# Optimization experiments

Hardware: AMD Instinct MI355X
Metric: run time of the kernel (lower is better)

## Reference

```python
import jax, jax.numpy as jnp
import numpy as np

B, C, L = 128, 1, 4096


def setup_inputs() -> dict:
    key = jax.random.key(0)
    x_0 = jax.random.normal(key, (B, C, L), dtype=jnp.float32)
    return {"x_0": x_0}


def reference(x_0):
    # Original: per-sample F.conv1d(x, flip(x), padding=L-1).
    # Cross-correlation with a flipped kernel == full linear convolution:
    #   out[b, t] = sum_c sum_i x[b,c,i] * x[b,c,t-i],  t in [0, 2L-2]
    # Vectorized over batch and channels via vmap; summed over channels
    # (conv1d contracts input channels against the weight's channel dim).
    conv = jax.vmap(jax.vmap(lambda a: jnp.convolve(a, a, mode='full')))(x_0)  # [B, C, 2L-1]
    return conv.sum(axis=1)[:, None, :]  # [B, 1, 2L-1]
```

## Files before the change

### kernel.cpp

```cpp
#include <hip/hip_runtime.h>

#define LL    4096
#define OUTL  8191
#define FPAD  272
#define NPDW  2336
#define CB1   2352
#define RB    4704
#define BTOP  5887
#define LDSDW 9824

typedef short v8s __attribute__((ext_vector_type(8)));
typedef float v4f __attribute__((ext_vector_type(4)));

__device__ __forceinline__ unsigned bf16b(float f) {
    unsigned u = __builtin_bit_cast(unsigned, f);
    u += 0x7fff + ((u >> 16) & 1);
    return u >> 16;
}
__device__ __forceinline__ unsigned pk(float lo, float hi) {
    return bf16b(lo) | (bf16b(hi) << 16);
}
__device__ __forceinline__ int swz(int g) {
    return (g & ~15) | ((g & 1) << 3) | ((g & 15) >> 1);
}

struct Frag {
    unsigned x0, x1, x2, x3, y0, y1, y2, y3;
    uint4 b3, b2, b1, b0;
};

__global__ __launch_bounds__(512, 4)
void selfconv_mfma7(const float* __restrict__ xg, float* __restrict__ outg) {
    __shared__ unsigned lds[LDSDW];
    const int tid = threadIdx.x;
    const int blk = blockIdx.x;
    const int b   = blk & 127;
    const int id  = blk >> 7;
    const int rg  = (id == 0) ? 0 : (id == 1) ? 3 : (id == 2) ? 1 : 2;
    const int T0  = rg << 11;
    const float* __restrict__ xb = xg + b * LL;

#pragma unroll
    for (int rr = 0; rr < 2; ++rr) {
        int w = tid + rr * 512;
        if (w < 584) {
            int E = 8 * w - FPAD;
            float e0,e1,e2,e3,e4,e5,e6,e7,e8;
            if (E >= 0 && E + 8 < LL) {
                float4 fa = *(const float4*)(xb + E);
                float4 fb = *(const float4*)(xb + E + 4);
                e0=fa.x; e1=fa.y; e2=fa.z; e3=fa.w;
                e4=fb.x; e5=fb.y; e6=fb.z; e7=fb.w; e8=xb[E+8];
            } else {
                float t[9];
#pragma unroll
                for (int k = 0; k < 9; ++k) {
                    int e = E + k;
                    t[k] = (e >= 0 && e < LL) ? xb[e] : 0.f;
                }
                e0=t[0]; e1=t[1]; e2=t[2]; e3=t[3]; e4=t[4];
                e5=t[5]; e6=t[6]; e7=t[7]; e8=t[8];
            }
            uint4 d0{pk(e0,e1), pk(e2,e3), pk(e4,e5), pk(e6,e7)};
            uint4 d1{pk(e1,e2), pk(e3,e4), pk(e5,e6), pk(e7,e8)};
            *(uint4*)&lds[4 * w]       = d0;
            *(uint4*)&lds[CB1 + 4 * w] = d1;
        }
    }
    {
        int g = 224 + tid;
        int x0 = BTOP - 7 - 8 * g;
        float4 fa = *(const float4*)(xb + x0);
        float4 fb = *(const float4*)(xb + x0 + 4);
        uint4 o{pk(fb.w, fb.z), pk(fb.y, fb.x), pk(fa.w, fa.z), pk(fa.y, fa.x)};
        *(uint4*)&lds[RB + 4 * swz(g)] = o;
    }
    if (tid < 480) {
        int u = (tid < 224) ? tid : tid + 512;
        *(uint4*)&lds[RB + 4 * u] = uint4{0, 0, 0, 0};
    }
    __syncthreads();

    const int wv = tid >> 6, lane = tid & 63, ln16 = lane & 15, q = lane >> 4;

    int mn = 0x7fffffff, mx = -0x7fffffff;
#pragma unroll
    for (int u = 0; u < 2; ++u)
#pragma unroll
        for (int v = 0; v < 4; ++v) {
            int base = T0 + 256 * u + 512 * v;
            int iLo = base - (LL - 1); if (iLo < 0) iLo = 0;
            int iHi = base + 255;      if (iHi > LL - 1) iHi = LL - 1;
            int a = iLo - 256 * u; if (a < mn) mn = a;
            int c2 = iHi - 256 * u; if (c2 > mx) mx = c2;
        }
    const int base_   = mn - 15;
    const int i0start = base_ - ((base_ - 1) & 7);
    const int nch     = ((mx - i0start) >> 5) + 1;
    const int nw      = (nch - wv + 7) >> 3;
    const int i0w     = i0start + 32 * wv;

    const int s0p = i0w + ln16 + 8 * q + FPAD;
    const int aw  = (s0p >> 1) + ((s0p & 1) ? CB1 : 0);
    const int g3 = (4352 - T0 + i0w - 16 * ln16 + 8 * q) >> 3;
    const int bw = RB + 4 * swz(g3);

    v4f a00{0,0,0,0}, a01{0,0,0,0}, a02{0,0,0,0}, a03{0,0,0,0};
    v4f a10{0,0,0,0}, a11{0,0,0,0}, a12{0,0,0,0}, a13{0,0,0,0};

    auto ld = [&](Frag& F, int a, int w) {
        F.x0 = lds[a];       F.x1 = lds[a + 1];
        F.x2 = lds[a + 2];   F.x3 = lds[a + 3];
        F.y0 = lds[a + 128]; F.y1 = lds[a + 129];
        F.y2 = lds[a + 130]; F.y3 = lds[a + 131];
        F.b3 = *(const uint4*)&lds[w];
        F.b2 = *(const uint4*)&lds[w + 256];
        F.b1 = *(const uint4*)&lds[w + 512];
        F.b0 = *(const uint4*)&lds[w + 768];
    };
    auto mkA = [](unsigned u0, unsigned u1, unsigned u2, unsigned u3) {
        union { unsigned x[4]; v8s s; } z;
        z.x[0] = u0; z.x[1] = u1; z.x[2] = u2; z.x[3] = u3; return z.s;
    };
    auto mkB = [](uint4 v) {
        union { unsigned x[4]; v8s s; } z;
        z.x[0] = v.x; z.x[1] = v.y; z.x[2] = v.z; z.x[3] = v.w; return z.s;
    };
    auto cmp = [&](const Frag& F) {
        v8s A0 = mkA(F.x0, F.x1, F.x2, F.x3);
        v8s A1 = mkA(F.y0, F.y1, F.y2, F.y3);
        v8s B3 = mkB(F.b3), B2 = mkB(F.b2), B1 = mkB(F.b1), B0 = mkB(F.b0);
        a03 = __builtin_amdgcn_mfma_f32_16x16x32_bf16(A0, B3, a03, 0, 0, 0);
        a13 = __builtin_amdgcn_mfma_f32_16x16x32_bf16(A1, B3, a13, 0, 0, 0);
        a02 = __builtin_amdgcn_mfma_f32_16x16x32_bf16(A0, B2, a02, 0, 0, 0);
        a12 = __builtin_amdgcn_mfma_f32_16x16x32_bf16(A1, B2, a12, 0, 0, 0);
        a01 = __builtin_amdgcn_mfma_f32_16x16x32_bf16(A0, B1, a01, 0, 0, 0);
        a11 = __builtin_amdgcn_mfma_f32_16x16x32_bf16(A1, B1, a11, 0, 0, 0);
        a00 = __builtin_amdgcn_mfma_f32_16x16x32_bf16(A0, B0, a00, 0, 0, 0);
        a10 = __builtin_amdgcn_mfma_f32_16x16x32_bf16(A1, B0, a10, 0, 0, 0);
    };

    Frag F0, F1;
    int awE = aw, bwE = bw, awO = aw + 128, bwO = bw + 128;
    ld(F0, awE, bwE); awE += 256; bwE += 256;
    ld(F1, awO, bwO); awO += 256; bwO += 256;
    int c = 0;
    for (; c + 2 < nw; c += 2) {
        cmp(F0); ld(F0, awE, bwE); awE += 256; bwE += 256;
        cmp(F1); ld(F1, awO, bwO); awO += 256; bwO += 256;
    }
    cmp(F0);
    if (c + 1 < nw) cmp(F1);

    float* fs = (float*)lds;
    __syncthreads();
    if (wv >= 4) {
        int sb = (wv - 4) * 2304 + lane * 36;
        *(v4f*)&fs[sb]      = a00; *(v4f*)&fs[sb + 4]  = a10;
        *(v4f*)&fs[sb + 8]  = a01; *(v4f*)&fs[sb + 12] = a11;
        *(v4f*)&fs[sb + 16] = a02; *(v4f*)&fs[sb + 20] = a12;
        *(v4f*)&fs[sb + 24] = a03; *(v4f*)&fs[sb + 28] = a13;
    }
    __syncthreads();
    if (wv < 4) {
        int sb = wv * 2304 + lane * 36;
        a00 += *(const v4f*)&fs[sb];      a10 += *(const v4f*)&fs[sb + 4];
        a01 += *(const v4f*)&fs[sb + 8];  a11 += *(const v4f*)&fs[sb + 12];
        a02 += *(const v4f*)&fs[sb + 16]; a12 += *(const v4f*)&fs[sb + 20];
        a03 += *(const v4f*)&fs[sb + 24]; a13 += *(const v4f*)&fs[sb + 28];
    }
    __syncthreads();
    if (wv >= 1 && wv < 4) {
        int sb = (wv - 1) * 2304 + lane * 36;
        *(v4f*)&fs[sb]      = a00; *(v4f*)&fs[sb + 4]  = a10;
        *(v4f*)&fs[sb + 8]  = a01; *(v4f*)&fs[sb + 12] = a11;
        *(v4f*)&fs[sb + 16] = a02; *(v4f*)&fs[sb + 20] = a12;
        *(v4f*)&fs[sb + 24] = a03; *(v4f*)&fs[sb + 28] = a13;
    }
    __syncthreads();
    if (wv == 0) {
#pragma unroll
        for (int s = 0; s < 3; ++s) {
            int sb = s * 2304 + lane * 36;
            a00 += *(const v4f*)&fs[sb];      a10 += *(const v4f*)&fs[sb + 4];
            a01 += *(const v4f*)&fs[sb + 8];  a11 += *(const v4f*)&fs[sb + 12];
            a02 += *(const v4f*)&fs[sb + 16]; a12 += *(const v4f*)&fs[sb + 20];
            a03 += *(const v4f*)&fs[sb + 24]; a13 += *(const v4f*)&fs[sb + 28];
        }
        float* __restrict__ ob = outg + b * OUTL;
        const v4f* accs[8] = {&a00, &a10, &a01, &a11, &a02, &a12, &a03, &a13};
#pragma unroll
        for (int uv = 0; uv < 8; ++uv) {
            int u = uv & 1, v = uv >> 1;
            int tilebase = T0 + 256 * u + 512 * v;
            int tb = tilebase + 4 * q + 16 * ln16;
            v4f a = *accs[uv];
            if (tilebase + 255 < OUTL) {
                *(v4f*)&ob[tb] = a;
            } else {
#pragma unroll
                for (int r2 = 0; r2 < 4; ++r2)
                    if (tb + r2 < OUTL) ob[tb + r2] = a[r2];
            }
        }
    }
}

extern "C" void kernel_launch(void* const* d_in, const int* in_sizes, int n_in,
                              void* d_out, int out_size, void* d_ws, size_t ws_size,
                              hipStream_t stream) {
    const float* x = (const float*)d_in[0];
    float* out = (float*)d_out;
    selfconv_mfma7<<<dim3(512), dim3(512), 0, stream>>>(x, out);
}
```

Before: 61.95 us.

## Split output into 1024-wide ranges across 1024 blocks with fewer accumulators

Result: no change. 62.00 us (+0.1%).

```diff
diff --git a/kernel.cpp b/kernel.cpp
--- a/kernel.cpp
+++ b/kernel.cpp
@@ -5,9 +5,9 @@
 #define FPAD  272
 #define NPDW  2336
 #define CB1   2352
-#define RB    4704
+#define RB    4688
 #define BTOP  5887
-#define LDSDW 9824
+#define LDSDW 8656
 
 typedef short v8s __attribute__((ext_vector_type(8)));
 typedef float v4f __attribute__((ext_vector_type(4)));
@@ -24,20 +24,16 @@
     return (g & ~15) | ((g & 1) << 3) | ((g & 15) >> 1);
 }
 
-struct Frag {
-    unsigned x0, x1, x2, x3, y0, y1, y2, y3;
-    uint4 b3, b2, b1, b0;
-};
-
-__global__ __launch_bounds__(512, 4)
-void selfconv_mfma7(const float* __restrict__ xg, float* __restrict__ outg) {
+__global__ __launch_bounds__(512, 8)
+void selfconv_mfma8(const float* __restrict__ xg, float* __restrict__ outg) {
     __shared__ unsigned lds[LDSDW];
     const int tid = threadIdx.x;
     const int blk = blockIdx.x;
     const int b   = blk & 127;
     const int id  = blk >> 7;
-    const int rg  = (id == 0) ? 0 : (id == 1) ? 3 : (id == 2) ? 1 : 2;
-    const int T0  = rg << 11;
+    const int perm[8] = {0, 3, 1, 2, 5, 6, 4, 7};
+    const int rg  = perm[id];
+    const int T0  = rg << 10;
     const float* __restrict__ xb = xg + b * LL;
 
 #pragma unroll
@@ -87,7 +83,7 @@
 #pragma unroll
     for (int u = 0; u < 2; ++u)
 #pragma unroll
-        for (int v = 0; v < 4; ++v) {
+        for (int v = 0; v < 2; ++v) {
             int base = T0 + 256 * u + 512 * v;
             int iLo = base - (LL - 1); if (iLo < 0) iLo = 0;
             int iHi = base + 255;      if (iHi > LL - 1) iHi = LL - 1;
@@ -101,23 +97,12 @@
     const int i0w     = i0start + 32 * wv;
 
     const int s0p = i0w + ln16 + 8 * q + FPAD;
-    const int aw  = (s0p >> 1) + ((s0p & 1) ? CB1 : 0);
-    const int g3 = (4352 - T0 + i0w - 16 * ln16 + 8 * q) >> 3;
-    const int bw = RB + 4 * swz(g3);
+    int aw = (s0p >> 1) + ((s0p & 1) ? CB1 : 0);
+    const int g1 = (BTOP - T0 - 512 - 16 * ln16 + i0w + 8 * q) >> 3;
+    int bw = RB + 4 * swz(g1);
 
-    v4f a00{0,0,0,0}, a01{0,0,0,0}, a02{0,0,0,0}, a03{0,0,0,0};
-    v4f a10{0,0,0,0}, a11{0,0,0,0}, a12{0,0,0,0}, a13{0,0,0,0};
+    v4f a00{0,0,0,0}, a10{0,0,0,0}, a01{0,0,0,0}, a11{0,0,0,0};
 
-    auto ld = [&](Frag& F, int a, int w) {
-        F.x0 = lds[a];       F.x1 = lds[a + 1];
-        F.x2 = lds[a + 2];   F.x3 = lds[a + 3];
-        F.y0 = lds[a + 128]; F.y1 = lds[a + 129];
-        F.y2 = lds[a + 130]; F.y3 = lds[a + 131];
-        F.b3 = *(const uint4*)&lds[w];
-        F.b2 = *(const uint4*)&lds[w + 256];
-        F.b1 = *(const uint4*)&lds[w + 512];
-        F.b0 = *(const uint4*)&lds[w + 768];
-    };
     auto mkA = [](unsigned u0, unsigned u1, unsigned u2, unsigned u3) {
         union { unsigned x[4]; v8s s; } z;
         z.x[0] = u0; z.x[1] = u1; z.x[2] = u2; z.x[3] = u3; return z.s;
@@ -126,75 +111,57 @@
         union { unsigned x[4]; v8s s; } z;
         z.x[0] = v.x; z.x[1] = v.y; z.x[2] = v.z; z.x[3] = v.w; return z.s;
     };
-    auto cmp = [&](const Frag& F) {
-        v8s A0 = mkA(F.x0, F.x1, F.x2, F.x3);
-        v8s A1 = mkA(F.y0, F.y1, F.y2, F.y3);
-        v8s B3 = mkB(F.b3), B2 = mkB(F.b2), B1 = mkB(F.b1), B0 = mkB(F.b0);
-        a03 = __builtin_amdgcn_mfma_f32_16x16x32_bf16(A0, B3, a03, 0, 0, 0);
-        a13 = __builtin_amdgcn_mfma_f32_16x16x32_bf16(A1, B3, a13, 0, 0, 0);
-        a02 = __builtin_amdgcn_mfma_f32_16x16x32_bf16(A0, B2, a02, 0, 0, 0);
-        a12 = __builtin_amdgcn_mfma_f32_16x16x32_bf16(A1, B2, a12, 0, 0, 0);
+
+    for (int c = 0; c < nw; ++c) {
+        unsigned x0 = lds[aw],       x1 = lds[aw + 1];
+        unsigned x2 = lds[aw + 2],   x3 = lds[aw + 3];
+        unsigned y0 = lds[aw + 128], y1 = lds[aw + 129];
+        unsigned y2 = lds[aw + 130], y3 = lds[aw + 131];
+        uint4 bv1 = *(const uint4*)&lds[bw];
+        uint4 bv0 = *(const uint4*)&lds[bw + 256];
+        v8s A0 = mkA(x0, x1, x2, x3);
+        v8s A1 = mkA(y0, y1, y2, y3);
+        v8s B1 = mkB(bv1);
+        v8s B0 = mkB(bv0);
+        a00 = __builtin_amdgcn_mfma_f32_16x16x32_bf16(A0, B0, a00, 0, 0, 0);
+        a10 = __builtin_amdgcn_mfma_f32_16x16x32_bf16(A1, B0, a10, 0, 0, 0);
         a01 = __builtin_amdgcn_mfma_f32_16x16x32_bf16(A0, B1, a01, 0, 0, 0);
         a11 = __builtin_amdgcn_mfma_f32_16x16x32_bf16(A1, B1, a11, 0, 0, 0);
-        a00 = __builtin_amdgcn_mfma_f32_16x16x32_bf16(A0, B0, a00, 0, 0, 0);
-        a10 = __builtin_amdgcn_mfma_f32_16x16x32_bf16(A1, B0, a10, 0, 0, 0);
-    };
-
-    Frag F0, F1;
-    int awE = aw, bwE = bw, awO = aw + 128, bwO = bw + 128;
-    ld(F0, awE, bwE); awE += 256; bwE += 256;
-    ld(F1, awO, bwO); awO += 256; bwO += 256;
-    int c = 0;
-    for (; c + 2 < nw; c += 2) {
-        cmp(F0); ld(F0, awE, bwE); awE += 256; bwE += 256;
-        cmp(F1); ld(F1, awO, bwO); awO += 256; bwO += 256;
+        aw += 128; bw += 128;
     }
-    cmp(F0);
-    if (c + 1 < nw) cmp(F1);
 
     float* fs = (float*)lds;
-    __syncthreads();
-    if (wv >= 4) {
-        int sb = (wv - 4) * 2304 + lane * 36;
+    auto dump = [&](int slot) {
+        int sb = slot * 1280 + lane * 20;
         *(v4f*)&fs[sb]      = a00; *(v4f*)&fs[sb + 4]  = a10;
         *(v4f*)&fs[sb + 8]  = a01; *(v4f*)&fs[sb + 12] = a11;
-        *(v4f*)&fs[sb + 16] = a02; *(v4f*)&fs[sb + 20] = a12;
-        *(v4f*)&fs[sb + 24] = a03; *(v4f*)&fs[sb + 28] = a13;
-    }
-    __syncthreads();
-    if (wv < 4) {
-        int sb = wv * 2304 + lane * 36;
+    };
+    auto gather = [&](int slot) {
+        int sb = slot * 1280 + lane * 20;
         a00 += *(const v4f*)&fs[sb];      a10 += *(const v4f*)&fs[sb + 4];
         a01 += *(const v4f*)&fs[sb + 8];  a11 += *(const v4f*)&fs[sb + 12];
-        a02 += *(const v4f*)&fs[sb + 16]; a12 += *(const v4f*)&fs[sb + 20];
-        a03 += *(const v4f*)&fs[sb + 24]; a13 += *(const v4f*)&fs[sb + 28];
-    }
+    };
     __syncthreads();
-    if (wv >= 1 && wv < 4) {
-        int sb = (wv - 1) * 2304 + lane * 36;
-        *(v4f*)&fs[sb]      = a00; *(v4f*)&fs[sb + 4]  = a10;
-        *(v4f*)&fs[sb + 8]  = a01; *(v4f*)&fs[sb + 12] = a11;
-        *(v4f*)&fs[sb + 16] = a02; *(v4f*)&fs[sb + 20] = a12;
-        *(v4f*)&fs[sb + 24] = a03; *(v4f*)&fs[sb + 28] = a13;
-    }
+    if (wv >= 4) dump(wv - 4);
+    __syncthreads();
+    if (wv < 4) gather(wv);
+    __syncthreads();
+    if (wv == 2 || wv == 3) dump(wv - 2);
+    __syncthreads();
+    if (wv < 2) gather(wv);
+    __syncthreads();
+    if (wv == 1) dump(0);
     __syncthreads();
     if (wv == 0) {
+        gather(0);
+        float* __restrict__ ob = outg + b * OUTL;
+        const v4f* accs[4] = {&a00, &a10, &a01, &a11};
+        const int offs[4]  = {0, 256, 512, 768};
 #pragma unroll
-        for (int s = 0; s < 3; ++s) {
-            int sb = s * 2304 + lane * 36;
-            a00 += *(const v4f*)&fs[sb];      a10 += *(const v4f*)&fs[sb + 4];
-            a01 += *(const v4f*)&fs[sb + 8];  a11 += *(const v4f*)&fs[sb + 12];
-            a02 += *(const v4f*)&fs[sb + 16]; a12 += *(const v4f*)&fs[sb + 20];
-            a03 += *(const v4f*)&fs[sb + 24]; a13 += *(const v4f*)&fs[sb + 28];
-        }
-        float* __restrict__ ob = outg + b * OUTL;
-        const v4f* accs[8] = {&a00, &a10, &a01, &a11, &a02, &a12, &a03, &a13};
-#pragma unroll
-        for (int uv = 0; uv < 8; ++uv) {
-            int u = uv & 1, v = uv >> 1;
-            int tilebase = T0 + 256 * u + 512 * v;
+        for (int t4 = 0; t4 < 4; ++t4) {
+            int tilebase = T0 + offs[t4];
             int tb = tilebase + 4 * q + 16 * ln16;
-            v4f a = *accs[uv];
+            v4f a = *accs[t4];
             if (tilebase + 255 < OUTL) {
                 *(v4f*)&ob[tb] = a;
             } else {
@@ -211,5 +178,5 @@
                               hipStream_t stream) {
     const float* x = (const float*)d_in[0];
     float* out = (float*)d_out;
-    selfconv_mfma7<<<dim3(512), dim3(512), 0, stream>>>(x, out);
+    selfconv_mfma8<<<dim3(1024), dim3(512), 0, stream>>>(x, out);
 }
```
